# Kernel tuning notes

Hardware: AMD Instinct MI355X
Metric: run time of the kernel (lower is better)

The kernel has to match this reference:

```python
import jax, jax.numpy as jnp
import numpy as np

B, NQ, D, NH, DH = 16, 300, 256, 8, 32
L, P, FFN = 3, 4, 1024
LEVEL_SHAPES = [(80, 80), (40, 40), (20, 20)]
S = sum(h * w for h, w in LEVEL_SHAPES)  # 8400
EPS = 1e-5

PARAM_NAMES = ['wq', 'bq', 'wk', 'bk', 'wv', 'bv', 'wo', 'bo', 'ln1_g', 'ln1_b',
               'w_off', 'b_off', 'w_aw', 'b_aw', 'w_val', 'b_val', 'w_out', 'b_out',
               'ln2_g', 'ln2_b', 'w_fc1', 'b_fc1', 'w_fc2', 'b_fc2', 'ln3_g', 'ln3_b']


def _ln(x, g, b):
    m = jnp.mean(x, -1, keepdims=True)
    v = jnp.mean(jnp.square(x - m), -1, keepdims=True)
    return (x - m) * jax.lax.rsqrt(v + EPS) * g + b


def _bilinear(v_l, loc, Hl, Wl):
    # v_l: [B, Hl*Wl, NH, DH]; loc in [0,1]: [B, NQ, NH, P, 2]
    # matches torch grid_sample(align_corners=False, padding='zeros') with grid=2*loc-1
    x = loc[..., 0] * Wl - 0.5
    y = loc[..., 1] * Hl - 0.5
    x0 = jnp.floor(x)
    y0 = jnp.floor(y)
    vt = v_l.transpose(0, 2, 1, 3)  # [B, NH, Sl, DH]
    out = jnp.zeros((v_l.shape[0], NQ, NH, P, DH), v_l.dtype)
    for dx in (0, 1):
        for dy in (0, 1):
            xi = x0 + dx
            yi = y0 + dy
            w = (1.0 - jnp.abs(x - xi)) * (1.0 - jnp.abs(y - yi))
            valid = (xi >= 0) & (xi < Wl) & (yi >= 0) & (yi < Hl)
            idx = (jnp.clip(yi, 0, Hl - 1) * Wl + jnp.clip(xi, 0, Wl - 1)).astype(jnp.int32)
            idx_t = idx.transpose(0, 2, 1, 3).reshape(idx.shape[0], NH, NQ * P)
            g = jnp.take_along_axis(vt, idx_t[..., None], axis=2)  # [B, NH, NQ*P, DH]
            g = g.reshape(-1, NH, NQ, P, DH).transpose(0, 2, 1, 3, 4)
            out = out + g * (w * valid)[..., None]
    return out  # [B, NQ, NH, P, DH]


def _forward(hidden_states, pos_embed, encoder_hidden_states, reference_points, spatial_shapes, p):
    h = hidden_states
    # ---- self-attention (pos added to q and k only) ----
    hp = h + pos_embed
    q = (hp @ p['wq'] + p['bq']).reshape(B, NQ, NH, DH)
    k = (hp @ p['wk'] + p['bk']).reshape(B, NQ, NH, DH)
    v = (h @ p['wv'] + p['bv']).reshape(B, NQ, NH, DH)
    scores = jnp.einsum('bqhd,bkhd->bhqk', q, k) * (1.0 / np.sqrt(DH).astype(np.float32))
    attn = jax.nn.softmax(scores, -1)
    sa = jnp.einsum('bhqk,bkhd->bqhd', attn, v).reshape(B, NQ, D) @ p['wo'] + p['bo']
    h = _ln(h + sa, p['ln1_g'], p['ln1_b'])

    # ---- multiscale deformable cross-attention ----
    hp = h + pos_embed
    value = (encoder_hidden_states @ p['w_val'] + p['b_val']).reshape(B, S, NH, DH)
    off = (hp @ p['w_off'] + p['b_off']).reshape(B, NQ, NH, L, P, 2)
    aw = jax.nn.softmax((hp @ p['w_aw'] + p['b_aw']).reshape(B, NQ, NH, L * P), -1)
    aw = aw.reshape(B, NQ, NH, L, P)
    normalizer = jnp.stack([spatial_shapes[:, 1], spatial_shapes[:, 0]], -1).astype(h.dtype)  # [L,2] = (W,H)
    loc = reference_points[:, :, None, :, None, :] + off / normalizer[None, None, None, :, None, :]
    out = jnp.zeros((B, NQ, NH, DH), h.dtype)
    start = 0
    for l, (Hl, Wl) in enumerate(LEVEL_SHAPES):
        v_l = value[:, start:start + Hl * Wl]
        sampled = _bilinear(v_l, loc[:, :, :, l], Hl, Wl)  # [B,NQ,NH,P,DH]
        out = out + jnp.sum(sampled * aw[:, :, :, l, :, None], axis=3)
        start += Hl * Wl
    ca = out.reshape(B, NQ, D) @ p['w_out'] + p['b_out']
    h = _ln(h + ca, p['ln2_g'], p['ln2_b'])

    # ---- MLP ----
    mlp = jax.nn.relu(h @ p['w_fc1'] + p['b_fc1']) @ p['w_fc2'] + p['b_fc2']
    return _ln(h + mlp, p['ln3_g'], p['ln3_b'])


def setup_inputs() -> dict:
    key = jax.random.key(0)
    ks = iter(jax.random.split(key, 48))
    def nrm(shape, s=0.02):
        return jax.random.normal(next(ks), shape, jnp.float32) * s
    inp = {
        'hidden_states': jax.random.normal(next(ks), (B, NQ, D), jnp.float32),
        'pos_embed': jax.random.normal(next(ks), (B, NQ, D), jnp.float32),
        'encoder_hidden_states': jax.random.normal(next(ks), (B, S, D), jnp.float32),
        'reference_points': jax.random.uniform(next(ks), (B, NQ, L, 2), jnp.float32),
        'spatial_shapes': jnp.array(LEVEL_SHAPES, jnp.int32),
        'wq': nrm((D, D)), 'bq': jnp.zeros(D),
        'wk': nrm((D, D)), 'bk': jnp.zeros(D),
        'wv': nrm((D, D)), 'bv': jnp.zeros(D),
        'wo': nrm((D, D)), 'bo': jnp.zeros(D),
        'ln1_g': jnp.ones(D), 'ln1_b': jnp.zeros(D),
        'w_off': nrm((D, NH * L * P * 2)), 'b_off': nrm((NH * L * P * 2,), 0.1),
        'w_aw': nrm((D, NH * L * P)), 'b_aw': jnp.zeros(NH * L * P),
        'w_val': nrm((D, D)), 'b_val': jnp.zeros(D),
        'w_out': nrm((D, D)), 'b_out': jnp.zeros(D),
        'ln2_g': jnp.ones(D), 'ln2_b': jnp.zeros(D),
        'w_fc1': nrm((D, FFN)), 'b_fc1': jnp.zeros(FFN),
        'w_fc2': nrm((FFN, D)), 'b_fc2': jnp.zeros(D),
        'ln3_g': jnp.ones(D), 'ln3_b': jnp.zeros(D),
    }
    return inp


def reference(hidden_states, pos_embed, encoder_hidden_states, reference_points, spatial_shapes,
              wq, bq, wk, bk, wv, bv, wo, bo, ln1_g, ln1_b,
              w_off, b_off, w_aw, b_aw, w_val, b_val, w_out, b_out,
              ln2_g, ln2_b, w_fc1, b_fc1, w_fc2, b_fc2, ln3_g, ln3_b):
    p = dict(wq=wq, bq=bq, wk=wk, bk=bk, wv=wv, bv=bv, wo=wo, bo=bo,
             ln1_g=ln1_g, ln1_b=ln1_b, w_off=w_off, b_off=b_off, w_aw=w_aw, b_aw=b_aw,
             w_val=w_val, b_val=b_val, w_out=w_out, b_out=b_out, ln2_g=ln2_g, ln2_b=ln2_b,
             w_fc1=w_fc1, b_fc1=b_fc1, w_fc2=w_fc2, b_fc2=b_fc2, ln3_g=ln3_g, ln3_b=ln3_b)
    return _forward(hidden_states, pos_embed, encoder_hidden_states, reference_points, spatial_shapes, p)
```

## Files before the change

kernel.cpp:

```cpp
#include <hip/hip_runtime.h>
#include <hip/hip_bf16.h>
#include <math.h>

#define B_   16
#define NQ_  300
#define D_   256
#define NH_  8
#define DH_  32
#define L_   3
#define P_   4
#define FFN_ 1024
#define S_   8400
#define ROWS_ (B_*NQ_)
#define NB_   (ROWS_*D_)

typedef __attribute__((ext_vector_type(4))) unsigned short ushort4_t;
typedef __attribute__((ext_vector_type(8))) unsigned short ushort8_t;
typedef __attribute__((ext_vector_type(8))) short bf16x8;
typedef __attribute__((ext_vector_type(4))) float f32x4;

__device__ inline unsigned short f2b(float f) {
    __hip_bfloat16 h = __float2bfloat16(f);
    return __builtin_bit_cast(unsigned short, h);
}
__device__ inline float b2f(unsigned short u) {
    union { unsigned u; float f; } c; c.u = ((unsigned)u) << 16; return c.f;
}

__global__ __launch_bounds__(256) void prep_kernel(
    const float* __restrict__ wq, const float* __restrict__ wk,
    const float* __restrict__ wv, const float* __restrict__ wo,
    const float* __restrict__ w_val, const float* __restrict__ w_out,
    const float* __restrict__ w_off, const float* __restrict__ w_aw,
    const float* __restrict__ w_fc1, const float* __restrict__ w_fc2,
    const float* __restrict__ bq, const float* __restrict__ bk,
    const float* __restrict__ b_off, const float* __restrict__ b_aw,
    unsigned short* __restrict__ wtqk, unsigned short* __restrict__ wtv,
    unsigned short* __restrict__ wto, unsigned short* __restrict__ wtval,
    unsigned short* __restrict__ wtout, unsigned short* __restrict__ wtoa,
    unsigned short* __restrict__ wtfc1, unsigned short* __restrict__ wtfc2,
    float* __restrict__ bqk, float* __restrict__ boa)
{
    const int bid = blockIdx.x;
    if (bid >= 968) {
        int idx = (bid - 968)*256 + threadIdx.x;
        if (idx < 512) bqk[idx] = (idx < 256) ? bq[idx] : bk[idx-256];
        else { int j = idx - 512; if (j < 288) boa[j] = (j < 192) ? b_off[j] : b_aw[j-192]; }
        return;
    }
    const float* src; unsigned short* dst; int K, N, t;
    if      (bid < 64)  { src=wq;    dst=wtqk;         K=256;  N=256;  t=bid; }
    else if (bid < 128) { src=wk;    dst=wtqk+65536;   K=256;  N=256;  t=bid-64; }
    else if (bid < 192) { src=wv;    dst=wtv;          K=256;  N=256;  t=bid-128; }
    else if (bid < 256) { src=wo;    dst=wto;          K=256;  N=256;  t=bid-192; }
    else if (bid < 320) { src=w_val; dst=wtval;        K=256;  N=256;  t=bid-256; }
    else if (bid < 384) { src=w_out; dst=wtout;        K=256;  N=256;  t=bid-320; }
    else if (bid < 432) { src=w_off; dst=wtoa;         K=256;  N=192;  t=bid-384; }
    else if (bid < 456) { src=w_aw;  dst=wtoa+49152;   K=256;  N=96;   t=bid-432; }
    else if (bid < 712) { src=w_fc1; dst=wtfc1;        K=256;  N=1024; t=bid-456; }
    else                { src=w_fc2; dst=wtfc2;        K=1024; N=256;  t=bid-712; }

    __shared__ unsigned short tl[32][33];
    int tid = threadIdx.x;
    int tx = tid & 31, ty = tid >> 5;
    int ntx = N >> 5;
    int n0 = (t % ntx) * 32, k0 = (t / ntx) * 32;
    #pragma unroll
    for (int i = 0; i < 4; ++i)
        tl[tx][ty + i*8] = f2b(src[(size_t)(k0 + ty + i*8)*N + n0 + tx]);
    __syncthreads();
    #pragma unroll
    for (int i = 0; i < 4; ++i)
        dst[(size_t)(n0 + ty + i*8)*K + k0 + tx] = tl[ty + i*8][tx];
}

#define GEMM_PREAMBLE()                                                        \
    const int tid  = threadIdx.x;                                              \
    const int lane = tid & 63;                                                 \
    const int w    = tid >> 6;                                                 \
    const int wr   = w >> 1, wc = w & 1;                                       \
    const int m0   = blockIdx.y * 64;                                          \
    const int n0   = blockIdx.x * 128;                                         \
    const int fr   = lane & 15, fq = lane >> 4;                                \
    const int arow = tid >> 2, aseg = (tid & 3) * 8;                           \
    const int brow = tid >> 1, bseg = (tid & 1) * 16;                          \
    const bool a_ok = (m0 + arow) < M;                                         \
    const bool b_ok = (n0 + brow) < N;                                         \
    const float*          aptr  = A  + (size_t)(m0 + arow)*K + aseg;           \
    const float*          aptr2 = A2 ? A2 + (size_t)(m0 + arow)*K + aseg : (const float*)0; \
    const unsigned short* bptr  = WT + (size_t)(n0 + brow)*K + bseg;           \
    f32x4 acc[2][4];                                                           \
    _Pragma("unroll") for (int m = 0; m < 2; ++m)                              \
        _Pragma("unroll") for (int n = 0; n < 4; ++n)                          \
            acc[m][n] = (f32x4){0.f, 0.f, 0.f, 0.f};                           \
    float4 avA0, avB0, avA1, avB1;                                             \
    ushort8_t bvA0, bvB0, bvA1, bvB1;

#define GEMM_LOAD(avA, avB, bvA, bvB, kk) do {                                 \
    if (a_ok) {                                                                \
        avA = *(const float4*)(aptr + (kk));                                   \
        avB = *(const float4*)(aptr + (kk) + 4);                               \
        if (aptr2) {                                                           \
            float4 x2 = *(const float4*)(aptr2 + (kk));                        \
            float4 y2 = *(const float4*)(aptr2 + (kk) + 4);                    \
            avA.x += x2.x; avA.y += x2.y; avA.z += x2.z; avA.w += x2.w;        \
            avB.x += y2.x; avB.y += y2.y; avB.z += y2.z; avB.w += y2.w;        \
        }                                                                      \
    } else { avA = (float4){0,0,0,0}; avB = (float4){0,0,0,0}; }               \
    if (b_ok) { bvA = *(const ushort8_t*)(bptr + (kk));                        \
                bvB = *(const ushort8_t*)(bptr + (kk) + 8); }                  \
    else { _Pragma("unroll") for (int j = 0; j < 8; ++j){bvA[j]=0;bvB[j]=0;} } \
} while (0)

#define GEMM_STORE_LDS(avA, avB, bvA, bvB) do {                                \
    ushort8_t ac;                                                              \
    ac[0]=f2b(avA.x); ac[1]=f2b(avA.y); ac[2]=f2b(avA.z); ac[3]=f2b(avA.w);    \
    ac[4]=f2b(avB.x); ac[5]=f2b(avB.y); ac[6]=f2b(avB.z); ac[7]=f2b(avB.w);    \
    *(ushort8_t*)&As[arow][aseg]     = ac;                                     \
    *(ushort8_t*)&Bs[brow][bseg]     = bvA;                                    \
    *(ushort8_t*)&Bs[brow][bseg + 8] = bvB;                                    \
} while (0)

#define GEMM_COMPUTE() do {                                                    \
    bf16x8 af[2], bfv[4];                                                      \
    _Pragma("unroll") for (int m = 0; m < 2; ++m)                              \
        af[m] = *(const bf16x8*)&As[wr*32 + m*16 + fr][fq*8];                  \
    _Pragma("unroll") for (int n = 0; n < 4; ++n)                              \
        bfv[n] = *(const bf16x8*)&Bs[wc*64 + n*16 + fr][fq*8];                 \
    _Pragma("unroll") for (int m = 0; m < 2; ++m)                              \
        _Pragma("unroll") for (int n = 0; n < 4; ++n)                          \
            acc[m][n] = __builtin_amdgcn_mfma_f32_16x16x32_bf16(               \
                af[m], bfv[n], acc[m][n], 0, 0, 0);                            \
} while (0)

#define GEMM_KLOOP()                                                           \
    GEMM_LOAD(avA0, avB0, bvA0, bvB0, 0);                                      \
    for (int k0 = 0; k0 < K; k0 += 64) {                                       \
        __syncthreads();                                                       \
        GEMM_STORE_LDS(avA0, avB0, bvA0, bvB0);                                \
        GEMM_LOAD(avA1, avB1, bvA1, bvB1, k0 + 32);                            \
        __syncthreads();                                                       \
        GEMM_COMPUTE();                                                        \
        __syncthreads();                                                       \
        GEMM_STORE_LDS(avA1, avB1, bvA1, bvB1);                                \
        if (k0 + 64 < K) GEMM_LOAD(avA0, avB0, bvA0, bvB0, k0 + 64);           \
        __syncthreads();                                                       \
        GEMM_COMPUTE();                                                        \
    }

__global__ __launch_bounds__(256) void gemm_mfma64(
    const float* __restrict__ A, const float* __restrict__ A2,
    const unsigned short* __restrict__ WT,
    const float* __restrict__ bias, float* __restrict__ C,
    int M, int N, int K, int relu)
{
    __shared__ unsigned short As[64][40];
    __shared__ unsigned short Bs[128][40];
    GEMM_PREAMBLE();
    GEMM_KLOOP();

    #pragma unroll
    for (int n = 0; n < 4; ++n) {
        int col = n0 + wc*64 + n*16 + fr;
        if (col < N) {
            float bcol = bias[col];
            #pragma unroll
            for (int m = 0; m < 2; ++m) {
                int rbase = m0 + wr*32 + m*16 + fq*4;
                #pragma unroll
                for (int r = 0; r < 4; ++r) {
                    int row = rbase + r;
                    if (row < M) {
                        float vv = acc[m][n][r] + bcol;
                        if (relu) vv = fmaxf(vv, 0.f);
                        C[(size_t)row * N + col] = vv;
                    }
                }
            }
        }
    }
}

__global__ __launch_bounds__(256) void stage1_kernel(
    const float* __restrict__ ehs, const float* __restrict__ h_in,
    const float* __restrict__ pos,
    const unsigned short* __restrict__ wtval, const float* __restrict__ b_val,
    unsigned short* __restrict__ val_bf,
    const unsigned short* __restrict__ wtqk, const float* __restrict__ bqk,
    float* __restrict__ buf_qk,
    const unsigned short* __restrict__ wtv, const float* __restrict__ bv,
    float* __restrict__ buf_v)
{
    __shared__ unsigned short As[64][40];
    __shared__ unsigned short Bs[128][40];

    const int bid = blockIdx.x;
    int path, m0, n0, Ncols = 256;
    const float* Ap; const float* A2p = nullptr;
    const unsigned short* Bp; const float* bias; float* C = nullptr;
    if (bid < 4200) {
        path = 0; m0 = (bid >> 1)*64; n0 = (bid & 1)*128;
        Ap = ehs; Bp = wtval; bias = b_val;
    } else if (bid < 4500) {
        int t = bid - 4200;
        path = 1; m0 = (t >> 2)*64; n0 = (t & 3)*128;
        Ap = h_in; A2p = pos; Bp = wtqk; bias = bqk; C = buf_qk; Ncols = 512;
    } else {
        int t = bid - 4500;
        path = 2; m0 = (t >> 1)*64; n0 = (t & 1)*128;
        Ap = h_in; Bp = wtv; bias = bv; C = buf_v;
    }

    const int tid  = threadIdx.x;
    const int lane = tid & 63;
    const int w    = tid >> 6;
    const int wr   = w >> 1, wc = w & 1;
    const int fr   = lane & 15, fq = lane >> 4;
    const int arow = tid >> 2, aseg = (tid & 3) * 8;
    const int brow = tid >> 1, bseg = (tid & 1) * 16;
    const bool a_ok = true, b_ok = true;
    const int K = 256;
    const float*          aptr  = Ap + (size_t)(m0 + arow)*256 + aseg;
    const float*          aptr2 = A2p ? A2p + (size_t)(m0 + arow)*256 + aseg : (const float*)0;
    const unsigned short* bptr  = Bp + (size_t)(n0 + brow)*256 + bseg;

    f32x4 acc[2][4];
    #pragma unroll
    for (int m = 0; m < 2; ++m)
        #pragma unroll
        for (int n = 0; n < 4; ++n)
            acc[m][n] = (f32x4){0.f, 0.f, 0.f, 0.f};
    float4 avA0, avB0, avA1, avB1;
    ushort8_t bvA0, bvB0, bvA1, bvB1;

    GEMM_KLOOP();

    if (path == 0) {
        #pragma unroll
        for (int n = 0; n < 4; ++n) {
            int col = n0 + wc*64 + n*16 + fr;
            int hh = col >> 5, dd = col & 31;
            float bcol = bias[col];
            #pragma unroll
            for (int m = 0; m < 2; ++m) {
                int rbase = m0 + wr*32 + m*16 + fq*4;
                #pragma unroll
                for (int r = 0; r < 4; ++r) {
                    unsigned row = rbase + r;
                    unsigned bb = row / (unsigned)S_;
                    unsigned ss = row - bb * (unsigned)S_;
                    val_bf[((size_t)(bb*NH_ + hh)*S_ + ss)*DH_ + dd] = f2b(acc[m][n][r] + bcol);
                }
            }
        }
    } else {
        #pragma unroll
        for (int n = 0; n < 4; ++n) {
            int col = n0 + wc*64 + n*16 + fr;
            float bcol = bias[col];
            #pragma unroll
            for (int m = 0; m < 2; ++m) {
                int rbase = m0 + wr*32 + m*16 + fq*4;
                #pragma unroll
                for (int r = 0; r < 4; ++r)
                    C[(size_t)(rbase + r) * Ncols + col] = acc[m][n][r] + bcol;
            }
        }
    }
}

__global__ __launch_bounds__(256) void gemm_relu_bf16(
    const float* __restrict__ A, const unsigned short* __restrict__ WT,
    const float* __restrict__ bias, unsigned short* __restrict__ OUT,
    int M, int N, int K)
{
    __shared__ unsigned short As[64][40];
    __shared__ unsigned short Bs[128][40];
    const float* A2 = nullptr;
    GEMM_PREAMBLE();
    GEMM_KLOOP();

    #pragma unroll
    for (int n = 0; n < 4; ++n) {
        int col = n0 + wc*64 + n*16 + fr;
        float bcol = bias[col];
        #pragma unroll
        for (int m = 0; m < 2; ++m) {
            int rbase = m0 + wr*32 + m*16 + fq*4;
            #pragma unroll
            for (int r = 0; r < 4; ++r)
                OUT[(size_t)(rbase + r) * N + col] = f2b(fmaxf(acc[m][n][r] + bcol, 0.f));
        }
    }
}

#define GLN16_COMPUTE() do {                                                   \
    bf16x8 af = *(const bf16x8*)&As[fr][fq*8];                                 \
    _Pragma("unroll") for (int n = 0; n < 4; ++n) {                            \
        bf16x8 bfv = *(const bf16x8*)&Bs[w*64 + n*16 + fr][fq*8];              \
        acc[n] = __builtin_amdgcn_mfma_f32_16x16x32_bf16(af, bfv, acc[n], 0, 0, 0); \
    }                                                                          \
} while (0)

#define GLN16_EPILOGUE()                                                       \
    float gcol[4], bcol2[4], biascol[4];                                       \
    _Pragma("unroll") for (int n = 0; n < 4; ++n) {                            \
        int col = w*64 + n*16 + fr;                                            \
        biascol[n] = bias[col]; gcol[n] = g[col]; bcol2[n] = bb[col];          \
    }                                                                          \
    _Pragma("unroll") for (int r = 0; r < 4; ++r) {                            \
        int row = fq*4 + r;                                                    \
        float s = 0.f, sq = 0.f;                                               \
        _Pragma("unroll") for (int n = 0; n < 4; ++n) {                        \
            int col = w*64 + n*16 + fr;                                        \
            float vv = acc[n][r] + biascol[n]                                  \
                     + X[(size_t)(m0 + row)*256 + col];                        \
            acc[n][r] = vv; s += vv; sq += vv*vv;                              \
        }                                                                      \
        s  += __shfl_xor(s, 1);  sq += __shfl_xor(sq, 1);                      \
        s  += __shfl_xor(s, 2);  sq += __shfl_xor(sq, 2);                      \
        s  += __shfl_xor(s, 4);  sq += __shfl_xor(sq, 4);                      \
        s  += __shfl_xor(s, 8);  sq += __shfl_xor(sq, 8);                      \
        if (fr == 0) { psum[row][w] = s; psq[row][w] = sq; }                   \
    }                                                                          \
    __syncthreads();                                                           \
    _Pragma("unroll") for (int r = 0; r < 4; ++r) {                            \
        int row = fq*4 + r;                                                    \
        float mean = (psum[row][0]+psum[row][1]+psum[row][2]+psum[row][3]) * (1.0f/256.0f); \
        float ex2  = (psq[row][0]+psq[row][1]+psq[row][2]+psq[row][3]) * (1.0f/256.0f);     \
        float rstd = rsqrtf(ex2 - mean*mean + 1e-5f);                          \
        _Pragma("unroll") for (int n = 0; n < 4; ++n) {                        \
            int col = w*64 + n*16 + fr;                                        \
            OUT[(size_t)(m0 + row)*256 + col] =                                \
                (acc[n][r] - mean)*rstd*gcol[n] + bcol2[n];                    \
        }                                                                      \
    }

__global__ __launch_bounds__(256) void gemm_ln_f32A(
    const float* __restrict__ A, const unsigned short* __restrict__ WT,
    const float* __restrict__ bias, const float* __restrict__ X,
    const float* __restrict__ g, const float* __restrict__ bb,
    float* __restrict__ OUT, int K)
{
    __shared__ unsigned short As[16][40];
    __shared__ unsigned short Bs[256][40];
    __shared__ float psum[16][4], psq[16][4];

    const int tid  = threadIdx.x;
    const int lane = tid & 63;
    const int w    = tid >> 6;
    const int m0   = blockIdx.x * 16;
    const int fr   = lane & 15, fq = lane >> 4;
    const bool astage = tid < 64;
    const int arow = (tid >> 2) & 15, aseg = (tid & 3) * 8;
    const float*          aptr = A  + (size_t)(m0 + arow)*K + aseg;
    const unsigned short* bptr = WT + (size_t)tid*K;

    f32x4 acc[4];
    #pragma unroll
    for (int n = 0; n < 4; ++n) acc[n] = (f32x4){0.f, 0.f, 0.f, 0.f};

    float4 a0x = {0,0,0,0}, a0y = {0,0,0,0}, a1x = {0,0,0,0}, a1y = {0,0,0,0};
    ushort8_t b0[4], b1[4];

    if (astage) { a0x = *(const float4*)(aptr); a0y = *(const float4*)(aptr + 4); }
    #pragma unroll
    for (int j = 0; j < 4; ++j) b0[j] = *(const ushort8_t*)(bptr + j*8);
    for (int k0 = 0; k0 < K; k0 += 64) {
        __syncthreads();
        if (astage) {
            ushort8_t ac;
            ac[0]=f2b(a0x.x); ac[1]=f2b(a0x.y); ac[2]=f2b(a0x.z); ac[3]=f2b(a0x.w);
            ac[4]=f2b(a0y.x); ac[5]=f2b(a0y.y); ac[6]=f2b(a0y.z); ac[7]=f2b(a0y.w);
            *(ushort8_t*)&As[arow][aseg] = ac;
        }
        #pragma unroll
        for (int j = 0; j < 4; ++j) *(ushort8_t*)&Bs[tid][j*8] = b0[j];
        if (astage) { a1x = *(const float4*)(aptr + k0 + 32); a1y = *(const float4*)(aptr + k0 + 36); }
        #pragma unroll
        for (int j = 0; j < 4; ++j) b1[j] = *(const ushort8_t*)(bptr + k0 + 32 + j*8);
        __syncthreads();
        GLN16_COMPUTE();
        __syncthreads();
        if (astage) {
            ushort8_t ac;
            ac[0]=f2b(a1x.x); ac[1]=f2b(a1x.y); ac[2]=f2b(a1x.z); ac[3]=f2b(a1x.w);
            ac[4]=f2b(a1y.x); ac[5]=f2b(a1y.y); ac[6]=f2b(a1y.z); ac[7]=f2b(a1y.w);
            *(ushort8_t*)&As[arow][aseg] = ac;
        }
        #pragma unroll
        for (int j = 0; j < 4; ++j) *(ushort8_t*)&Bs[tid][j*8] = b1[j];
        if (k0 + 64 < K) {
            if (astage) { a0x = *(const float4*)(aptr + k0 + 64); a0y = *(const float4*)(aptr + k0 + 68); }
            #pragma unroll
            for (int j = 0; j < 4; ++j) b0[j] = *(const ushort8_t*)(bptr + k0 + 64 + j*8);
        }
        __syncthreads();
        GLN16_COMPUTE();
    }

    GLN16_EPILOGUE();
}

__global__ __launch_bounds__(256) void gemm_ln_bf16A(
    const unsigned short* __restrict__ A, const unsigned short* __restrict__ WT,
    const float* __restrict__ bias, const float* __restrict__ X,
    const float* __restrict__ g, const float* __restrict__ bb,
    float* __restrict__ OUT, int K)
{
    __shared__ unsigned short As[16][40];
    __shared__ unsigned short Bs[256][40];
    __shared__ float psum[16][4], psq[16][4];

    const int tid  = threadIdx.x;
    const int lane = tid & 63;
    const int w    = tid >> 6;
    const int m0   = blockIdx.x * 16;
    const int fr   = lane & 15, fq = lane >> 4;
    const bool astage = tid < 64;
    const int arow = (tid >> 2) & 15, aseg = (tid & 3) * 8;
    const unsigned short* aptr = A  + (size_t)(m0 + arow)*K + aseg;
    const unsigned short* bptr = WT + (size_t)tid*K;

    f32x4 acc[4];
    #pragma unroll
    for (int n = 0; n < 4; ++n) acc[n] = (f32x4){0.f, 0.f, 0.f, 0.f};

    ushort8_t a0, a1, b0[4], b1[4];
    #pragma unroll
    for (int j = 0; j < 8; ++j) { a0[j] = 0; a1[j] = 0; }

    if (astage) a0 = *(const ushort8_t*)(aptr);
    #pragma unroll
    for (int j = 0; j < 4; ++j) b0[j] = *(const ushort8_t*)(bptr + j*8);
    for (int k0 = 0; k0 < K; k0 += 64) {
        __syncthreads();
        if (astage) *(ushort8_t*)&As[arow][aseg] = a0;
        #pragma unroll
        for (int j = 0; j < 4; ++j) *(ushort8_t*)&Bs[tid][j*8] = b0[j];
        if (astage) a1 = *(const ushort8_t*)(aptr + k0 + 32);
        #pragma unroll
        for (int j = 0; j < 4; ++j) b1[j] = *(const ushort8_t*)(bptr + k0 + 32 + j*8);
        __syncthreads();
        GLN16_COMPUTE();
        __syncthreads();
        if (astage) *(ushort8_t*)&As[arow][aseg] = a1;
        #pragma unroll
        for (int j = 0; j < 4; ++j) *(ushort8_t*)&Bs[tid][j*8] = b1[j];
        if (k0 + 64 < K) {
            if (astage) a0 = *(const ushort8_t*)(aptr + k0 + 64);
            #pragma unroll
            for (int j = 0; j < 4; ++j) b0[j] = *(const ushort8_t*)(bptr + k0 + 64 + j*8);
        }
        __syncthreads();
        GLN16_COMPUTE();
    }

    GLN16_EPILOGUE();
}

__global__ __launch_bounds__(256) void self_attn_kernel(
    const float* __restrict__ qk, const float* __restrict__ v,
    float* __restrict__ sa)
{
    __shared__ unsigned short k_sw[304*32];
    __shared__ unsigned short vt[32][312];
    __shared__ unsigned short p_all[4][16][312];

    const int bid  = blockIdx.x;
    const int part = bid % 5;
    const int bh   = bid / 5;
    const int h    = bh & 7;
    const int b    = bh >> 3;
    const int tid  = threadIdx.x;
    const int lane = tid & 63;
    const int w    = tid >> 6;
    const int g    = lane >> 4;
    const int fr   = lane & 15;

    const size_t qbase = (size_t)b*NQ_*512 + h*DH_;
    const size_t kbase = qbase + 256;
    const size_t vbase = (size_t)b*NQ_*D_ + h*DH_;
    const size_t sbase = (size_t)b*NQ_*D_ + h*DH_;

    for (int i = tid; i < 1216; i += 256) {
        int r = i >> 2, u = i & 3;
        ushort8_t kb;
        if (r < NQ_) {
            const float* p8 = qk + kbase + (size_t)r*512 + u*8;
            float4 a0 = *(const float4*)p8;
            float4 a1 = *(const float4*)(p8 + 4);
            kb[0]=f2b(a0.x); kb[1]=f2b(a0.y); kb[2]=f2b(a0.z); kb[3]=f2b(a0.w);
            kb[4]=f2b(a1.x); kb[5]=f2b(a1.y); kb[6]=f2b(a1.z); kb[7]=f2b(a1.w);
        } else {
            #pragma unroll
            for (int j = 0; j < 8; ++j) kb[j] = 0;
        }
        int su = u ^ ((r >> 1) & 3);
        *(ushort8_t*)&k_sw[r*32 + su*8] = kb;
    }
    for (int i = tid; i < 1216; i += 256) {
        int kk = i >> 2, u = i & 3;
        if (kk < NQ_) {
            const float* p8 = v + vbase + (size_t)kk*D_ + u*8;
            float4 a0 = *(const float4*)p8;
            float4 a1 = *(const float4*)(p8 + 4);
            float f[8] = {a0.x,a0.y,a0.z,a0.w,a1.x,a1.y,a1.z,a1.w};
            #pragma unroll
            for (int j = 0; j < 8; ++j) vt[u*8 + j][kk] = f2b(f[j]);
        } else {
            #pragma unroll
            for (int j = 0; j < 8; ++j) vt[u*8 + j][kk] = 0;
        }
    }
    __syncthreads();

    const int q0 = part*64 + w*16;
    const int qi = q0 + fr;
    bf16x8 qf;
    if (qi < NQ_) {
        const float scale = 0.17677669529663687f;
        const float* p8 = qk + qbase + (size_t)qi*512 + g*8;
        float4 a0 = *(const float4*)p8;
        float4 a1 = *(const float4*)(p8 + 4);
        qf[0]=(short)f2b(a0.x*scale); qf[1]=(short)f2b(a0.y*scale);
        qf[2]=(short)f2b(a0.z*scale); qf[3]=(short)f2b(a0.w*scale);
        qf[4]=(short)f2b(a1.x*scale); qf[5]=(short)f2b(a1.y*scale);
        qf[6]=(short)f2b(a1.z*scale); qf[7]=(short)f2b(a1.w*scale);
    } else {
        #pragma unroll
        for (int j = 0; j < 8; ++j) qf[j] = 0;
    }

    const int ksw_u = g ^ ((fr >> 1) & 3);
    f32x4 acc[19];
    #pragma unroll
    for (int t = 0; t < 19; ++t) acc[t] = (f32x4){0.f,0.f,0.f,0.f};
    #pragma unroll
    for (int t = 0; t < 19; ++t) {
        int row = t*16 + fr;
        bf16x8 kf = *(const bf16x8*)&k_sw[row*32 + ksw_u*8];
        acc[t] = __builtin_amdgcn_mfma_f32_16x16x32_bf16(kf, qf, acc[t], 0, 0, 0);
    }
    if (g == 3) acc[18] = (f32x4){-1e30f, -1e30f, -1e30f, -1e30f};

    float m = -1e30f;
    #pragma unroll
    for (int t = 0; t < 19; ++t) {
        #pragma unroll
        for (int r = 0; r < 4; ++r) m = fmaxf(m, acc[t][r]);
    }
    m = fmaxf(m, __shfl_xor(m, 16));
    m = fmaxf(m, __shfl_xor(m, 32));
    float lsum = 0.f;
    #pragma unroll
    for (int t = 0; t < 19; ++t) {
        #pragma unroll
        for (int r = 0; r < 4; ++r) {
            float e = __expf(acc[t][r] - m);
            acc[t][r] = e;
            lsum += e;
        }
    }
    lsum += __shfl_xor(lsum, 16);
    lsum += __shfl_xor(lsum, 32);
    float inv = 1.0f / lsum;

    #pragma unroll
    for (int t = 0; t < 19; ++t) {
        ushort4_t pw = { f2b(acc[t][0]*inv), f2b(acc[t][1]*inv),
                         f2b(acc[t][2]*inv), f2b(acc[t][3]*inv) };
        *(ushort4_t*)&p_all[w][fr][t*16 + g*4] = pw;
    }

    f32x4 o0 = (f32x4){0.f,0.f,0.f,0.f};
    f32x4 o1 = (f32x4){0.f,0.f,0.f,0.f};
    #pragma unroll
    for (int ks = 0; ks < 10; ++ks) {
        int kb = ks*32 + g*8;
        bf16x8 pf, vf0, vf1;
        if (kb < 304) {
            pf  = *(const bf16x8*)&p_all[w][fr][kb];
            vf0 = *(const bf16x8*)&vt[fr][kb];
            vf1 = *(const bf16x8*)&vt[16 + fr][kb];
        } else {
            #pragma unroll
            for (int j = 0; j < 8; ++j) { pf[j] = 0; vf0[j] = 0; vf1[j] = 0; }
        }
        o0 = __builtin_amdgcn_mfma_f32_16x16x32_bf16(pf, vf0, o0, 0, 0, 0);
        o1 = __builtin_amdgcn_mfma_f32_16x16x32_bf16(pf, vf1, o1, 0, 0, 0);
    }

    #pragma unroll
    for (int r = 0; r < 4; ++r) {
        int qo = q0 + g*4 + r;
        if (qo < NQ_) {
            sa[sbase + (size_t)qo*D_ + fr]      = o0[r];
            sa[sbase + (size_t)qo*D_ + 16 + fr] = o1[r];
        }
    }
}

__global__ __launch_bounds__(256) void deform_kernel(
    const unsigned short* __restrict__ value, const float* __restrict__ oa,
    const float* __restrict__ refp, float* __restrict__ dout)
{
    int gid = blockIdx.x*256 + threadIdx.x;
    int l16 = gid & 15;
    int grp = gid >> 4;
    int h = grp & 7;
    int bq = grp >> 3;
    int qq = bq % NQ_;
    int b  = bq / NQ_;
    int d0 = l16*2;

    const int starts[3] = {0, 6400, 8000};
    const int Hs[3] = {80, 40, 20};

    const float* offp = oa + (size_t)(b*NQ_+qq)*288 + h*24;
    const float* awp  = oa + (size_t)(b*NQ_+qq)*288 + 192 + h*12;
    const float* refq = refp + (size_t)(b*NQ_+qq)*(L_*2);
    const unsigned short* vb = value + ((size_t)(b*NH_ + h)*S_)*DH_ + d0;

    float av[12];
    float mx = -1e30f;
    #pragma unroll
    for (int i = 0; i < 12; ++i) { av[i] = awp[i]; mx = fmaxf(mx, av[i]); }
    float ssum = 0.f;
    #pragma unroll
    for (int i = 0; i < 12; ++i) { av[i] = __expf(av[i]-mx); ssum += av[i]; }
    float sinv = 1.f / ssum;

    float acc0 = 0.f, acc1 = 0.f;
    #pragma unroll
    for (int l = 0; l < L_; l++) {
        int Hl = Hs[l], Wl = Hs[l];
        float rx = refq[l*2+0], ry = refq[l*2+1];
        const unsigned short* vlb = vb + (size_t)starts[l]*DH_;
        #pragma unroll
        for (int p = 0; p < P_; p++) {
            float ox = offp[(l*P_+p)*2+0], oy = offp[(l*P_+p)*2+1];
            float a  = av[l*P_+p] * sinv;
            float x = (rx + ox/(float)Wl)*(float)Wl - 0.5f;
            float y = (ry + oy/(float)Hl)*(float)Hl - 0.5f;
            float x0 = floorf(x), y0 = floorf(y);
            #pragma unroll
            for (int dy = 0; dy < 2; dy++) {
                #pragma unroll
                for (int dx = 0; dx < 2; dx++) {
                    float xi = x0 + dx, yi = y0 + dy;
                    float wgt = (1.f - fabsf(x-xi))*(1.f - fabsf(y-yi));
                    bool valid = (xi >= 0.f) && (xi < (float)Wl) && (yi >= 0.f) && (yi < (float)Hl);
                    if (valid && wgt != 0.f) {
                        int ix = (int)xi, iy = (int)yi;
                        unsigned u = *(const unsigned*)(vlb + (size_t)(iy*Wl + ix)*DH_);
                        float aw2 = a * wgt;
                        acc0 += aw2 * b2f((unsigned short)(u & 0xffff));
                        acc1 += aw2 * b2f((unsigned short)(u >> 16));
                    }
                }
            }
        }
    }
    float2 o = { acc0, acc1 };
    *(float2*)&dout[(size_t)grp*32 + d0] = o;
}

extern "C" void kernel_launch(void* const* d_in, const int* in_sizes, int n_in,
                              void* d_out, int out_size, void* d_ws, size_t ws_size,
                              hipStream_t stream) {
    (void)in_sizes; (void)n_in; (void)out_size; (void)ws_size;
    const float* h_in  = (const float*)d_in[0];
    const float* pos   = (const float*)d_in[1];
    const float* ehs   = (const float*)d_in[2];
    const float* refp  = (const float*)d_in[3];
    const float* wq    = (const float*)d_in[5];
    const float* bq    = (const float*)d_in[6];
    const float* wk    = (const float*)d_in[7];
    const float* bk    = (const float*)d_in[8];
    const float* wv    = (const float*)d_in[9];
    const float* bv    = (const float*)d_in[10];
    const float* wo    = (const float*)d_in[11];
    const float* bo    = (const float*)d_in[12];
    const float* ln1g  = (const float*)d_in[13];
    const float* ln1b  = (const float*)d_in[14];
    const float* w_off = (const float*)d_in[15];
    const float* b_off = (const float*)d_in[16];
    const float* w_aw  = (const float*)d_in[17];
    const float* b_aw  = (const float*)d_in[18];
    const float* w_val = (const float*)d_in[19];
    const float* b_val = (const float*)d_in[20];
    const float* w_out = (const float*)d_in[21];
    const float* b_out = (const float*)d_in[22];
    const float* ln2g  = (const float*)d_in[23];
    const float* ln2b  = (const float*)d_in[24];
    const float* w_fc1 = (const float*)d_in[25];
    const float* b_fc1 = (const float*)d_in[26];
    const float* w_fc2 = (const float*)d_in[27];
    const float* b_fc2 = (const float*)d_in[28];
    const float* ln3g  = (const float*)d_in[29];
    const float* ln3b  = (const float*)d_in[30];
    float* out = (float*)d_out;

    float* ws = (float*)d_ws;
    float* buf_qk   = ws + 1*(size_t)NB_;
    float* buf_v    = ws + 3*(size_t)NB_;
    float* buf_sa   = ws + 4*(size_t)NB_;
    float* buf_h1   = ws + 6*(size_t)NB_;
    float* buf_h2   = ws + 7*(size_t)NB_;
    float* buf_oa   = ws + 8*(size_t)NB_;
    unsigned short* fc1_bf = (unsigned short*)(ws + 9*(size_t)NB_ + NB_/2);
    unsigned short* val_bf = (unsigned short*)(ws + 13*(size_t)NB_ + NB_/2);

    unsigned short* wtb = (unsigned short*)(ws + 27*(size_t)NB_ + NB_/2);
    unsigned short* wtqk  = wtb;
    unsigned short* wtv   = wtqk  + 131072;
    unsigned short* wto   = wtv   + 65536;
    unsigned short* wtval = wto   + 65536;
    unsigned short* wtout = wtval + 65536;
    unsigned short* wtoa  = wtout + 65536;
    unsigned short* wtfc1 = wtoa  + 73728;
    unsigned short* wtfc2 = wtfc1 + 262144;
    float* bqk = (float*)(wtfc2 + 262144);
    float* boa = bqk + 512;

    dim3 blk(256);

    prep_kernel<<<dim3(972), blk, 0, stream>>>(
        wq, wk, wv, wo, w_val, w_out, w_off, w_aw, w_fc1, w_fc2,
        bq, bk, b_off, b_aw,
        wtqk, wtv, wto, wtval, wtout, wtoa, wtfc1, wtfc2, bqk, boa);

    stage1_kernel<<<dim3(4650), blk, 0, stream>>>(
        ehs, h_in, pos, wtval, b_val, val_bf, wtqk, bqk, buf_qk, wtv, bv, buf_v);

    self_attn_kernel<<<dim3(B_*NH_*5), blk, 0, stream>>>(buf_qk, buf_v, buf_sa);
    gemm_ln_f32A<<<dim3(ROWS_/16), blk, 0, stream>>>(
        buf_sa, wto, bo, h_in, ln1g, ln1b, buf_h1, 256);
    gemm_mfma64<<<dim3(3, 75), blk, 0, stream>>>(buf_h1, pos, wtoa, boa, buf_oa, ROWS_, 288, D_, 0);
    deform_kernel<<<dim3(ROWS_*NH_*16/256), blk, 0, stream>>>(val_bf, buf_oa, refp, buf_v);
    gemm_ln_f32A<<<dim3(ROWS_/16), blk, 0, stream>>>(
        buf_v, wtout, b_out, buf_h1, ln2g, ln2b, buf_h2, 256);
    gemm_relu_bf16<<<dim3(8, 75), blk, 0, stream>>>(buf_h2, wtfc1, b_fc1, fc1_bf, ROWS_, FFN_, D_);
    gemm_ln_bf16A<<<dim3(ROWS_/16), blk, 0, stream>>>(
        fc1_bf, wtfc2, b_fc2, buf_h2, ln3g, ln3b, out, FFN_);
}
```

Baseline: 216.3 us.

## Split value projection into dedicated wide-tile GEMM kernel with K-half staging

Splits the fused stage1 kernel into a small QKV projection kernel and a dedicated value-projection GEMM. The new gemm_val gives each block a full 256-wide output tile over 64 rows and stages K in two 128-wide halves, so every A row is read and converted to bf16 once instead of twice. This is meant to halve the reads of the large encoder input and cut per-block loop overhead. The cost is much more shared memory (about 100 KB per block), which limits occupancy, plus no double buffering between loads and MFMA and one extra kernel launch.

```diff
diff --git a/kernel.cpp b/kernel.cpp
--- a/kernel.cpp
+++ b/kernel.cpp
@@ -181,11 +181,8 @@
     }
 }
 
-__global__ __launch_bounds__(256) void stage1_kernel(
-    const float* __restrict__ ehs, const float* __restrict__ h_in,
-    const float* __restrict__ pos,
-    const unsigned short* __restrict__ wtval, const float* __restrict__ b_val,
-    unsigned short* __restrict__ val_bf,
+__global__ __launch_bounds__(256) void qkv_kernel(
+    const float* __restrict__ h_in, const float* __restrict__ pos,
     const unsigned short* __restrict__ wtqk, const float* __restrict__ bqk,
     float* __restrict__ buf_qk,
     const unsigned short* __restrict__ wtv, const float* __restrict__ bv,
@@ -195,20 +192,16 @@
     __shared__ unsigned short Bs[128][40];
 
     const int bid = blockIdx.x;
-    int path, m0, n0, Ncols = 256;
-    const float* Ap; const float* A2p = nullptr;
-    const unsigned short* Bp; const float* bias; float* C = nullptr;
-    if (bid < 4200) {
-        path = 0; m0 = (bid >> 1)*64; n0 = (bid & 1)*128;
-        Ap = ehs; Bp = wtval; bias = b_val;
-    } else if (bid < 4500) {
-        int t = bid - 4200;
-        path = 1; m0 = (t >> 2)*64; n0 = (t & 3)*128;
-        Ap = h_in; A2p = pos; Bp = wtqk; bias = bqk; C = buf_qk; Ncols = 512;
+    int m0, n0, Ncols;
+    const float* A2p = nullptr;
+    const unsigned short* Bp; const float* bias; float* C;
+    if (bid < 300) {
+        m0 = (bid >> 2)*64; n0 = (bid & 3)*128;
+        A2p = pos; Bp = wtqk; bias = bqk; C = buf_qk; Ncols = 512;
     } else {
-        int t = bid - 4500;
-        path = 2; m0 = (t >> 1)*64; n0 = (t & 1)*128;
-        Ap = h_in; Bp = wtv; bias = bv; C = buf_v;
+        int t = bid - 300;
+        m0 = (t >> 1)*64; n0 = (t & 1)*128;
+        Bp = wtv; bias = bv; C = buf_v; Ncols = 256;
     }
 
     const int tid  = threadIdx.x;
@@ -220,7 +213,7 @@
     const int brow = tid >> 1, bseg = (tid & 1) * 16;
     const bool a_ok = true, b_ok = true;
     const int K = 256;
-    const float*          aptr  = Ap + (size_t)(m0 + arow)*256 + aseg;
+    const float*          aptr  = h_in + (size_t)(m0 + arow)*256 + aseg;
     const float*          aptr2 = A2p ? A2p + (size_t)(m0 + arow)*256 + aseg : (const float*)0;
     const unsigned short* bptr  = Bp + (size_t)(n0 + brow)*256 + bseg;
 
@@ -235,35 +228,96 @@
 
     GEMM_KLOOP();
 
-    if (path == 0) {
-        #pragma unroll
-        for (int n = 0; n < 4; ++n) {
-            int col = n0 + wc*64 + n*16 + fr;
-            int hh = col >> 5, dd = col & 31;
-            float bcol = bias[col];
-            #pragma unroll
-            for (int m = 0; m < 2; ++m) {
-                int rbase = m0 + wr*32 + m*16 + fq*4;
+    #pragma unroll
+    for (int n = 0; n < 4; ++n) {
+        int col = n0 + wc*64 + n*16 + fr;
+        float bcol = bias[col];
+        #pragma unroll
+        for (int m = 0; m < 2; ++m) {
+            int rbase = m0 + wr*32 + m*16 + fq*4;
+            #pragma unroll
+            for (int r = 0; r < 4; ++r)
+                C[(size_t)(rbase + r) * Ncols + col] = acc[m][n][r] + bcol;
+        }
+    }
+}
+
+__global__ __launch_bounds__(256) void gemm_val(
+    const float* __restrict__ A, const unsigned short* __restrict__ WT,
+    const float* __restrict__ bias, unsigned short* __restrict__ OUT)
+{
+    __shared__ unsigned short As4[4][64][40];
+    __shared__ unsigned short Bs4[4][256][40];
+
+    const int tid  = threadIdx.x;
+    const int lane = tid & 63;
+    const int w    = tid >> 6;
+    const int wr   = w >> 1, wc = w & 1;
+    const int m0   = blockIdx.x * 64;
+    const int fr   = lane & 15, fq = lane >> 4;
+
+    f32x4 acc[2][8];
+    #pragma unroll
+    for (int m = 0; m < 2; ++m)
+        #pragma unroll
+        for (int n = 0; n < 8; ++n)
+            acc[m][n] = (f32x4){0.f, 0.f, 0.f, 0.f};
+
+    for (int kh = 0; kh < 2; ++kh) {
+        const int kbase = kh * 128;
+        __syncthreads();
+        #pragma unroll
+        for (int i = 0; i < 4; ++i) {
+            int uf = i*256 + tid;
+            int row = uf >> 4, j = uf & 15;
+            const float* src = A + (size_t)(m0 + row)*256 + kbase + j*8;
+            float4 x = *(const float4*)src;
+            float4 y = *(const float4*)(src + 4);
+            ushort8_t u;
+            u[0]=f2b(x.x); u[1]=f2b(x.y); u[2]=f2b(x.z); u[3]=f2b(x.w);
+            u[4]=f2b(y.x); u[5]=f2b(y.y); u[6]=f2b(y.z); u[7]=f2b(y.w);
+            *(ushort8_t*)&As4[j>>2][row][(j&3)*8] = u;
+        }
+        #pragma unroll
+        for (int i = 0; i < 16; ++i) {
+            int uf = i*256 + tid;
+            int row = uf >> 4, j = uf & 15;
+            ushort8_t u = *(const ushort8_t*)(WT + (size_t)row*256 + kbase + j*8);
+            *(ushort8_t*)&Bs4[j>>2][row][(j&3)*8] = u;
+        }
+        __syncthreads();
+        #pragma unroll
+        for (int ks = 0; ks < 4; ++ks) {
+            bf16x8 af[2], bfv[8];
+            #pragma unroll
+            for (int m = 0; m < 2; ++m)
+                af[m] = *(const bf16x8*)&As4[ks][wr*32 + m*16 + fr][fq*8];
+            #pragma unroll
+            for (int n = 0; n < 8; ++n)
+                bfv[n] = *(const bf16x8*)&Bs4[ks][wc*128 + n*16 + fr][fq*8];
+            #pragma unroll
+            for (int m = 0; m < 2; ++m)
                 #pragma unroll
-                for (int r = 0; r < 4; ++r) {
-                    unsigned row = rbase + r;
-                    unsigned bb = row / (unsigned)S_;
-                    unsigned ss = row - bb * (unsigned)S_;
-                    val_bf[((size_t)(bb*NH_ + hh)*S_ + ss)*DH_ + dd] = f2b(acc[m][n][r] + bcol);
-                }
-            }
-        }
-    } else {
-        #pragma unroll
-        for (int n = 0; n < 4; ++n) {
-            int col = n0 + wc*64 + n*16 + fr;
-            float bcol = bias[col];
-            #pragma unroll
-            for (int m = 0; m < 2; ++m) {
-                int rbase = m0 + wr*32 + m*16 + fq*4;
-                #pragma unroll
-                for (int r = 0; r < 4; ++r)
-                    C[(size_t)(rbase + r) * Ncols + col] = acc[m][n][r] + bcol;
+                for (int n = 0; n < 8; ++n)
+                    acc[m][n] = __builtin_amdgcn_mfma_f32_16x16x32_bf16(
+                        af[m], bfv[n], acc[m][n], 0, 0, 0);
+        }
+    }
+
+    #pragma unroll
+    for (int n = 0; n < 8; ++n) {
+        int col = wc*128 + n*16 + fr;
+        int hh = col >> 5, dd = col & 31;
+        float bcol = bias[col];
+        #pragma unroll
+        for (int m = 0; m < 2; ++m) {
+            int rbase = m0 + wr*32 + m*16 + fq*4;
+            #pragma unroll
+            for (int r = 0; r < 4; ++r) {
+                unsigned row = rbase + r;
+                unsigned bb = row / (unsigned)S_;
+                unsigned ss = row - bb * (unsigned)S_;
+                OUT[((size_t)(bb*NH_ + hh)*S_ + ss)*DH_ + dd] = f2b(acc[m][n][r] + bcol);
             }
         }
     }
@@ -731,8 +785,9 @@
         bq, bk, b_off, b_aw,
         wtqk, wtv, wto, wtval, wtout, wtoa, wtfc1, wtfc2, bqk, boa);
 
-    stage1_kernel<<<dim3(4650), blk, 0, stream>>>(
-        ehs, h_in, pos, wtval, b_val, val_bf, wtqk, bqk, buf_qk, wtv, bv, buf_v);
+    qkv_kernel<<<dim3(450), blk, 0, stream>>>(
+        h_in, pos, wtqk, bqk, buf_qk, wtv, bv, buf_v);
+    gemm_val<<<dim3(2100), blk, 0, stream>>>(ehs, wtval, b_val, val_bf);
 
     self_attn_kernel<<<dim3(B_*NH_*5), blk, 0, stream>>>(buf_qk, buf_v, buf_sa);
     gemm_ln_f32A<<<dim3(ROWS_/16), blk, 0, stream>>>(
```

Result: slower. 220.8 us (+2.1%).
